# Kernel tuning notes

Hardware: AMD Instinct MI355X
Metric: run time of the kernel (lower is better)

## Reference

```python
import jax, jax.numpy as jnp
import numpy as np

N, E, IN_DIM, HID, HEADS = 50000, 400000, 128, 64, 4
NEG_SLOPE, LN_EPS = 0.2, 1e-5


def setup_inputs() -> dict:
    key = jax.random.key(0)
    ks = jax.random.split(key, 12)
    x = jax.random.normal(ks[0], (N, IN_DIM), dtype=jnp.float32)
    edge_index = jax.random.randint(ks[1], (2, E), 0, N, dtype=jnp.int64)
    s = 1.0 / np.sqrt(HID)
    return {
        "x": x,
        "edge_index": edge_index,
        "W_gcn": jax.random.normal(ks[2], (IN_DIM, HID), dtype=jnp.float32) / np.sqrt(IN_DIM),
        "b_gcn": jnp.zeros((HID,), dtype=jnp.float32),
        "W_gat": jax.random.normal(ks[3], (HID, HEADS * HID), dtype=jnp.float32) * s,
        "att_src": jax.random.normal(ks[4], (HEADS, HID), dtype=jnp.float32) * s,
        "att_dst": jax.random.normal(ks[5], (HEADS, HID), dtype=jnp.float32) * s,
        "b_gat": jnp.zeros((HID,), dtype=jnp.float32),
        "W_patch": jax.random.normal(ks[6], (HID, HID), dtype=jnp.float32) * s,
        "b_patch": jnp.zeros((HID,), dtype=jnp.float32),
        "gamma": jnp.ones((HID,), dtype=jnp.float32),
        "beta": jnp.zeros((HID,), dtype=jnp.float32),
    }


def _forward(x, edge_index, W_gcn, b_gcn, W_gat, att_src, att_dst, b_gat,
             W_patch, b_patch, gamma, beta):
    n = x.shape[0]
    loop = jnp.arange(n, dtype=edge_index.dtype)
    src = jnp.concatenate([edge_index[0], loop])  # self-loops appended (PyG default)
    dst = jnp.concatenate([edge_index[1], loop])

    # ---- GCNConv: symmetric degree normalization + scatter-add ----
    deg = jax.ops.segment_sum(jnp.ones_like(dst, dtype=jnp.float32), dst, num_segments=n)
    dinv = jnp.where(deg > 0, jax.lax.rsqrt(deg), 0.0)
    norm = dinv[src] * dinv[dst]  # [E+N]
    xw = x @ W_gcn  # [N,HID]
    h1 = jax.ops.segment_sum(xw[src] * norm[:, None], dst, num_segments=n) + b_gcn
    h1 = jax.nn.relu(h1)

    # ---- GATConv (heads=4, concat=False -> mean over heads) ----
    z = (h1 @ W_gat).reshape(n, HEADS, HID)  # [N,H,C]
    a_s = jnp.einsum('nhc,hc->nh', z, att_src)  # [N,H]
    a_d = jnp.einsum('nhc,hc->nh', z, att_dst)
    e = jax.nn.leaky_relu(a_s[src] + a_d[dst], negative_slope=NEG_SLOPE)  # [E+N,H]
    # segment-softmax over incoming edges per destination node
    m = jax.ops.segment_max(e, dst, num_segments=n)  # [N,H]
    ex = jnp.exp(e - m[dst])
    denom = jax.ops.segment_sum(ex, dst, num_segments=n)
    alpha = ex / denom[dst]  # [E+N,H]
    agg = jax.ops.segment_sum(z[src] * alpha[:, :, None], dst, num_segments=n)  # [N,H,C]
    h2 = jax.nn.relu(agg.mean(axis=1) + b_gat)

    # ---- residual fusion + LayerNorm (dropout is identity in eval) ----
    h_patch = h1 @ W_patch + b_patch
    h = h1 + h2 + h_patch
    mu = h.mean(axis=-1, keepdims=True)
    var = h.var(axis=-1, keepdims=True)
    return (h - mu) * jax.lax.rsqrt(var + LN_EPS) * gamma + beta


def reference(x, edge_index, W_gcn, b_gcn, W_gat, att_src, att_dst, b_gat,
              W_patch, b_patch, gamma, beta):
    return _forward(x, edge_index, W_gcn, b_gcn, W_gat, att_src, att_dst, b_gat,
                    W_patch, b_patch, gamma, beta)
```

## Files before the change

### kernel.cpp

```cpp
#include <hip/hip_runtime.h>
#include <math.h>

#define IN_DIM 128
#define HID 64
#define HEADS 4
#define NEG_SLOPE 0.2f
#define LN_EPS 1e-5f
#define ECAP 512

typedef short bf16x8 __attribute__((ext_vector_type(8)));
typedef float f32x4  __attribute__((ext_vector_type(4)));

__device__ inline unsigned short f2bf(float f) {
    unsigned u = __float_as_uint(f);
    u += 0x7fffu + ((u >> 16) & 1u);
    return (unsigned short)(u >> 16);
}
__device__ inline float bf2f(unsigned short s) {
    return __uint_as_float(((unsigned)s) << 16);
}
__device__ inline float leaky(float v) { return v > 0.0f ? v : NEG_SLOPE * v; }

__global__ void k_init_all(const unsigned long long* ei, int E, int n,
                           int* flag, int* hist,
                           const float* __restrict__ Wg, const float* __restrict__ Wp,
                           const float* __restrict__ Wgcn,
                           const float* __restrict__ att_s, const float* __restrict__ att_d,
                           unsigned short* __restrict__ Wt_post,
                           unsigned short* __restrict__ Wt_xw,
                           float* __restrict__ w_s, float* __restrict__ w_d) {
    int nzb = (n + 255) >> 8;
    int t = threadIdx.x;
    if ((int)blockIdx.x < nzb) {
        int i = blockIdx.x * 256 + t;
        if (i < n) hist[i] = 0;
        if (blockIdx.x == 0) {
            __shared__ int s_bad;
            if (t == 0) s_bad = 0;
            __syncthreads();
            int lim = E < 4096 ? E : 4096;
            int bad = 0;
            for (int k = t; k < lim; k += 256)
                if (ei[k] >= (unsigned long long)n) bad = 1;
            if (bad) s_bad = 1;
            __syncthreads();
            if (t == 0) *flag = s_bad ? 0 : 1;
        }
        return;
    }
    int role = blockIdx.x - nzb;
    if (role < 14) {
        int p = role * 256 + t;
        if (p < 2560) {
            int c = p & 63, kg = p >> 6;
            bf16x8 v;
#pragma unroll
            for (int j = 0; j < 8; j++) {
                int k = kg * 8 + j;
                float f;
                if (k < 256) f = 0.25f * Wg[(size_t)(k & 63) * 256 + (k >> 6) * 64 + c];
                else         f = Wp[(size_t)(k - 256) * 64 + c];
                v[j] = (short)f2bf(f);
            }
            *(bf16x8*)(&Wt_post[(size_t)p * 8]) = v;
        } else if (p < 2560 + 1024) {
            int q = p - 2560;
            int c = q & 63, kg = q >> 6;
            bf16x8 v;
#pragma unroll
            for (int j = 0; j < 8; j++)
                v[j] = (short)f2bf(Wgcn[(size_t)(kg * 8 + j) * 64 + c]);
            *(bf16x8*)(&Wt_xw[(size_t)q * 8]) = v;
        }
    } else {
        int h = t >> 6, k = t & 63;
        float ss = 0.0f, sd = 0.0f;
        for (int c = 0; c < HID; c++) {
            float w = Wg[(size_t)k * (HEADS * HID) + h * HID + c];
            ss += w * att_s[h * HID + c];
            sd += w * att_d[h * HID + c];
        }
        w_s[h * HID + k] = ss;
        w_d[h * HID + k] = sd;
    }
}

__global__ void k_hist(const void* ei, int E, const int* flag, int* hist) {
    int i = blockIdx.x * blockDim.x + threadIdx.x;
    if (i >= E) return;
    int is64 = *flag;
    int d;
    if (is64) d = (int)((const long long*)ei)[E + i];
    else      d = ((const int*)ei)[E + i];
    atomicAdd(&hist[d], 1);
}

__global__ __launch_bounds__(256) void k_scan1(const int* __restrict__ hist,
                                               int* __restrict__ tmp,
                                               int* __restrict__ partial, int n) {
    __shared__ int s[256];
    int t = threadIdx.x, i = blockIdx.x * 256 + t;
    int v = (i < n) ? hist[i] : 0;
    s[t] = v;
    __syncthreads();
    for (int off = 1; off < 256; off <<= 1) {
        int x = (t >= off) ? s[t - off] : 0;
        __syncthreads();
        s[t] += x;
        __syncthreads();
    }
    tmp[i] = s[t] - v;
    if (t == 255) partial[blockIdx.x] = s[255];
}

__global__ __launch_bounds__(256) void k_scan_apply(const int* __restrict__ tmp,
                                                    const int* __restrict__ partial,
                                                    const int* __restrict__ hist,
                                                    int* __restrict__ row_ptr,
                                                    int* __restrict__ cursor,
                                                    float* __restrict__ dinv,
                                                    int n, int nscan) {
    __shared__ int s[256];
    __shared__ int excl_s;
    int t = threadIdx.x;
    int v = (t < nscan) ? partial[t] : 0;
    s[t] = v;
    __syncthreads();
    for (int off = 1; off < 256; off <<= 1) {
        int x = (t >= off) ? s[t - off] : 0;
        __syncthreads();
        s[t] += x;
        __syncthreads();
    }
    if (t == 0) excl_s = (blockIdx.x == 0) ? 0 : s[blockIdx.x - 1];
    __syncthreads();
    int excl = excl_s;
    int i = blockIdx.x * 256 + t;
    if (i < n) {
        int v2 = tmp[i] + excl;
        row_ptr[i] = v2;
        cursor[i] = v2;
        dinv[i] = rsqrtf((float)(hist[i] + 1));
    }
}

__global__ __launch_bounds__(256) void k_scatter_xw(const void* ei, int E,
                                                    const int* __restrict__ flag,
                                                    int* __restrict__ cursor,
                                                    int* __restrict__ col,
                                                    const float* __restrict__ x,
                                                    const unsigned short* __restrict__ Wt_g,
                                                    const float* __restrict__ dinv,
                                                    unsigned short* __restrict__ xws, int n) {
    __shared__ unsigned short Wt[16 * 64 * 8];
    int nsb = (E + 255) >> 8;
    if ((int)blockIdx.x < nsb) {
        int i = blockIdx.x * 256 + threadIdx.x;
        if (i >= E) return;
        int is64 = *flag;
        int s, d;
        if (is64) { s = (int)((const long long*)ei)[i]; d = (int)((const long long*)ei)[E + i]; }
        else      { s = ((const int*)ei)[i];            d = ((const int*)ei)[E + i]; }
        int pos = atomicAdd(&cursor[d], 1);
        col[pos] = s;
    } else {
        int bx = blockIdx.x - nsb;
        int t = threadIdx.x;
        for (int idx = t; idx < 1024; idx += 256)
            *(bf16x8*)(&Wt[idx * 8]) = *(const bf16x8*)(&Wt_g[(size_t)idx * 8]);
        __syncthreads();
        int lane = t & 63;
        int li = lane & 15, quad = lane >> 4;
        int w = t >> 6;
        int r0 = bx * 64 + w * 16;
        int rload = r0 + li; if (rload > n - 1) rload = n - 1;
        f32x4 acc[4];
#pragma unroll
        for (int i = 0; i < 4; i++) acc[i] = (f32x4){0.f, 0.f, 0.f, 0.f};
        const float* xp = x + (size_t)rload * IN_DIM + quad * 8;
#pragma unroll
        for (int ks = 0; ks < 4; ks++) {
            float4 p0 = *(const float4*)(xp + ks * 32);
            float4 p1 = *(const float4*)(xp + ks * 32 + 4);
            bf16x8 a;
            a[0] = (short)f2bf(p0.x); a[1] = (short)f2bf(p0.y);
            a[2] = (short)f2bf(p0.z); a[3] = (short)f2bf(p0.w);
            a[4] = (short)f2bf(p1.x); a[5] = (short)f2bf(p1.y);
            a[6] = (short)f2bf(p1.z); a[7] = (short)f2bf(p1.w);
            int kg = ks * 4 + quad;
#pragma unroll
            for (int tt = 0; tt < 4; tt++) {
                bf16x8 bfr = *(const bf16x8*)(&Wt[((kg * 64) + tt * 16 + li) * 8]);
                acc[tt] = __builtin_amdgcn_mfma_f32_16x16x32_bf16(a, bfr, acc[tt], 0, 0, 0);
            }
        }
#pragma unroll
        for (int reg = 0; reg < 4; reg++) {
            int r = r0 + quad * 4 + reg;
            if (r >= n) continue;
            float dv = dinv[r];
#pragma unroll
            for (int tt = 0; tt < 4; tt++)
                xws[(size_t)r * HID + tt * 16 + li] = f2bf(acc[tt][reg] * dv);
        }
    }
}

__global__ __launch_bounds__(256) void k_gcn(const int* __restrict__ col,
                                             const int* __restrict__ row_ptr,
                                             const int* __restrict__ hist,
                                             const float* __restrict__ dinv,
                                             const unsigned short* __restrict__ xws,
                                             const float* __restrict__ b,
                                             const float* __restrict__ w_s,
                                             const float* __restrict__ w_d,
                                             unsigned short* __restrict__ h1b,
                                             float4* __restrict__ a_s,
                                             float4* __restrict__ a_d, int n) {
    int t = threadIdx.x, c = t & 63;
    int d = blockIdx.x * 4 + (t >> 6);
    if (d >= n) return;
    int start = row_ptr[d], cnt = hist[d];
    float acc = bf2f(xws[(size_t)d * HID + c]);
    int k = 0;
    for (; k + 3 < cnt; k += 4) {
        int s0 = col[start + k],     s1 = col[start + k + 1];
        int s2 = col[start + k + 2], s3 = col[start + k + 3];
        float v0 = bf2f(xws[(size_t)s0 * HID + c]);
        float v1 = bf2f(xws[(size_t)s1 * HID + c]);
        float v2 = bf2f(xws[(size_t)s2 * HID + c]);
        float v3 = bf2f(xws[(size_t)s3 * HID + c]);
        acc += (v0 + v1) + (v2 + v3);
    }
    for (; k < cnt; k++) acc += bf2f(xws[(size_t)col[start + k] * HID + c]);
    float h1c = fmaxf(acc * dinv[d] + b[c], 0.0f);
    h1b[(size_t)d * HID + c] = f2bf(h1c);
    float vs0 = h1c * w_s[c],       vs1 = h1c * w_s[64 + c];
    float vs2 = h1c * w_s[128 + c], vs3 = h1c * w_s[192 + c];
    float vd0 = h1c * w_d[c],       vd1 = h1c * w_d[64 + c];
    float vd2 = h1c * w_d[128 + c], vd3 = h1c * w_d[192 + c];
    for (int o = 32; o > 0; o >>= 1) {
        vs0 += __shfl_xor(vs0, o, 64); vs1 += __shfl_xor(vs1, o, 64);
        vs2 += __shfl_xor(vs2, o, 64); vs3 += __shfl_xor(vs3, o, 64);
        vd0 += __shfl_xor(vd0, o, 64); vd1 += __shfl_xor(vd1, o, 64);
        vd2 += __shfl_xor(vd2, o, 64); vd3 += __shfl_xor(vd3, o, 64);
    }
    if (c == 0) {
        a_s[d] = make_float4(vs0, vs1, vs2, vs3);
        a_d[d] = make_float4(vd0, vd1, vd2, vd3);
    }
}

__global__ __launch_bounds__(256) void k_attn(const int* __restrict__ col,
                                              const int* __restrict__ row_ptr,
                                              const int* __restrict__ hist,
                                              const float4* __restrict__ a_s,
                                              const float4* __restrict__ a_d,
                                              const unsigned short* __restrict__ h1b,
                                              unsigned short* __restrict__ X, int n) {
    __shared__ float4 wls[ECAP];
    __shared__ int    sls[ECAP];
    __shared__ int    sb[5];
    __shared__ float4 sad[4];
    int t = threadIdx.x;
    int d0 = blockIdx.x * 4;
    if (t == 0) {
        int bptr = row_ptr[d0];
        sb[0] = bptr;
        for (int j = 0; j < 4; j++) {
            int d = d0 + j;
            bptr += (d < n) ? hist[d] : 0;
            sb[j + 1] = bptr;
        }
    }
    if (t < 4 && d0 + t < n) sad[t] = a_d[d0 + t];
    __syncthreads();
    int start0 = sb[0];
    int totc = sb[4] - start0;
    int rel1 = sb[1] - start0, rel2 = sb[2] - start0, rel3 = sb[3] - start0;
    bool fast = (totc <= ECAP);
    if (fast) {
        for (int e = t; e < totc; e += 256) {
            int s = col[start0 + e];
            int j = (e >= rel1) + (e >= rel2) + (e >= rel3);
            float4 as = a_s[s], ad = sad[j];
            float4 w;
            w.x = __expf(leaky(as.x + ad.x));
            w.y = __expf(leaky(as.y + ad.y));
            w.z = __expf(leaky(as.z + ad.z));
            w.w = __expf(leaky(as.w + ad.w));
            wls[e] = w;
            sls[e] = s;
        }
    }
    __syncthreads();
    int c = t & 63, w = t >> 6;
    int d = d0 + w;
    if (d >= n) return;
    float4 ad = sad[w];
    float4 asd = a_s[d];
    float w0 = __expf(leaky(asd.x + ad.x));
    float w1 = __expf(leaky(asd.y + ad.y));
    float w2 = __expf(leaky(asd.z + ad.z));
    float w3 = __expf(leaky(asd.w + ad.w));
    float hs = bf2f(h1b[(size_t)d * HID + c]);
    float A0 = w0 * hs, A1 = w1 * hs, A2 = w2 * hs, A3 = w3 * hs;
    float l0 = w0, l1 = w1, l2 = w2, l3 = w3;
    int lo = sb[w] - start0, hi = sb[w + 1] - start0;
    if (fast) {
        int k = lo;
        for (; k + 3 < hi; k += 4) {
            int s0 = sls[k], s1 = sls[k + 1], s2 = sls[k + 2], s3 = sls[k + 3];
            float4 e0 = wls[k], e1 = wls[k + 1], e2 = wls[k + 2], e3 = wls[k + 3];
            float hv0 = bf2f(h1b[(size_t)s0 * HID + c]);
            float hv1 = bf2f(h1b[(size_t)s1 * HID + c]);
            float hv2 = bf2f(h1b[(size_t)s2 * HID + c]);
            float hv3 = bf2f(h1b[(size_t)s3 * HID + c]);
            A0 += e0.x * hv0 + e1.x * hv1 + e2.x * hv2 + e3.x * hv3;
            A1 += e0.y * hv0 + e1.y * hv1 + e2.y * hv2 + e3.y * hv3;
            A2 += e0.z * hv0 + e1.z * hv1 + e2.z * hv2 + e3.z * hv3;
            A3 += e0.w * hv0 + e1.w * hv1 + e2.w * hv2 + e3.w * hv3;
            l0 += (e0.x + e1.x) + (e2.x + e3.x);
            l1 += (e0.y + e1.y) + (e2.y + e3.y);
            l2 += (e0.z + e1.z) + (e2.z + e3.z);
            l3 += (e0.w + e1.w) + (e2.w + e3.w);
        }
        for (; k < hi; k++) {
            int s0 = sls[k];
            float4 e0 = wls[k];
            float hv0 = bf2f(h1b[(size_t)s0 * HID + c]);
            A0 += e0.x * hv0; l0 += e0.x;
            A1 += e0.y * hv0; l1 += e0.y;
            A2 += e0.z * hv0; l2 += e0.z;
            A3 += e0.w * hv0; l3 += e0.w;
        }
    } else {
        for (int k = lo; k < hi; k++) {
            int s0 = col[start0 + k];
            float4 as = a_s[s0];
            float u0 = __expf(leaky(as.x + ad.x));
            float u1 = __expf(leaky(as.y + ad.y));
            float u2 = __expf(leaky(as.z + ad.z));
            float u3 = __expf(leaky(as.w + ad.w));
            float hv0 = bf2f(h1b[(size_t)s0 * HID + c]);
            A0 += u0 * hv0; l0 += u0;
            A1 += u1 * hv0; l1 += u1;
            A2 += u2 * hv0; l2 += u2;
            A3 += u3 * hv0; l3 += u3;
        }
    }
    size_t base = (size_t)d * 256;
    X[base + c]       = f2bf(A0 / l0);
    X[base + 64 + c]  = f2bf(A1 / l1);
    X[base + 128 + c] = f2bf(A2 / l2);
    X[base + 192 + c] = f2bf(A3 / l3);
}

__global__ __launch_bounds__(256) void k_post(const unsigned short* __restrict__ Wt_g,
                                              const unsigned short* __restrict__ X,
                                              const unsigned short* __restrict__ h1b,
                                              const float* __restrict__ bp,
                                              const float* __restrict__ bg,
                                              const float* __restrict__ gamma,
                                              const float* __restrict__ beta,
                                              float* __restrict__ out, int n) {
    __shared__ unsigned short Wt[2560 * 8];
    int t = threadIdx.x;
    for (int idx = t; idx < 2560; idx += 256)
        *(bf16x8*)(&Wt[idx * 8]) = *(const bf16x8*)(&Wt_g[(size_t)idx * 8]);
    __syncthreads();

    int lane = t & 63;
    int li = lane & 15, quad = lane >> 4;
    int w = t >> 6;
    int rbase = blockIdx.x * 128 + w * 32;

    f32x4 acc_a[2][4], acc_h[2][4];
#pragma unroll
    for (int rt = 0; rt < 2; rt++)
#pragma unroll
        for (int i = 0; i < 4; i++) {
            acc_a[rt][i] = (f32x4){0.f, 0.f, 0.f, 0.f};
            acc_h[rt][i] = (f32x4){0.f, 0.f, 0.f, 0.f};
        }
#pragma unroll
    for (int ks = 0; ks < 10; ks++) {
        int kg = ks * 4 + quad;
        bf16x8 b0 = *(const bf16x8*)(&Wt[((kg * 64) + 0 * 16 + li) * 8]);
        bf16x8 b1 = *(const bf16x8*)(&Wt[((kg * 64) + 1 * 16 + li) * 8]);
        bf16x8 b2 = *(const bf16x8*)(&Wt[((kg * 64) + 2 * 16 + li) * 8]);
        bf16x8 b3 = *(const bf16x8*)(&Wt[((kg * 64) + 3 * 16 + li) * 8]);
#pragma unroll
        for (int rt = 0; rt < 2; rt++) {
            int row = rbase + rt * 16 + li;
            bf16x8 a;
            if (ks < 8)
                a = *(const bf16x8*)(X + (size_t)row * 256 + quad * 8 + ks * 32);
            else
                a = *(const bf16x8*)(h1b + (size_t)row * HID + quad * 8 + (ks - 8) * 32);
            if (ks < 8) {
                acc_a[rt][0] = __builtin_amdgcn_mfma_f32_16x16x32_bf16(a, b0, acc_a[rt][0], 0, 0, 0);
                acc_a[rt][1] = __builtin_amdgcn_mfma_f32_16x16x32_bf16(a, b1, acc_a[rt][1], 0, 0, 0);
                acc_a[rt][2] = __builtin_amdgcn_mfma_f32_16x16x32_bf16(a, b2, acc_a[rt][2], 0, 0, 0);
                acc_a[rt][3] = __builtin_amdgcn_mfma_f32_16x16x32_bf16(a, b3, acc_a[rt][3], 0, 0, 0);
            } else {
                acc_h[rt][0] = __builtin_amdgcn_mfma_f32_16x16x32_bf16(a, b0, acc_h[rt][0], 0, 0, 0);
                acc_h[rt][1] = __builtin_amdgcn_mfma_f32_16x16x32_bf16(a, b1, acc_h[rt][1], 0, 0, 0);
                acc_h[rt][2] = __builtin_amdgcn_mfma_f32_16x16x32_bf16(a, b2, acc_h[rt][2], 0, 0, 0);
                acc_h[rt][3] = __builtin_amdgcn_mfma_f32_16x16x32_bf16(a, b3, acc_h[rt][3], 0, 0, 0);
            }
        }
    }
    float bgv[4], bpv[4], gv[4], btv[4];
#pragma unroll
    for (int tt = 0; tt < 4; tt++) {
        int c = tt * 16 + li;
        bgv[tt] = bg[c]; bpv[tt] = bp[c]; gv[tt] = gamma[c]; btv[tt] = beta[c];
    }
#pragma unroll
    for (int rt = 0; rt < 2; rt++) {
#pragma unroll
        for (int reg = 0; reg < 4; reg++) {
            int r = rbase + rt * 16 + quad * 4 + reg;
            bool ok = (r < n);
            float hv[4];
            float s1 = 0.0f, s2 = 0.0f;
#pragma unroll
            for (int tt = 0; tt < 4; tt++) {
                int c = tt * 16 + li;
                float h1c = ok ? bf2f(h1b[(size_t)r * HID + c]) : 0.0f;
                float h2 = fmaxf(acc_a[rt][tt][reg] + bgv[tt], 0.0f);
                float h = h1c + h2 + acc_h[rt][tt][reg] + bpv[tt];
                hv[tt] = h;
                s1 += h; s2 += h * h;
            }
            for (int o = 8; o > 0; o >>= 1) {
                s1 += __shfl_xor(s1, o, 64);
                s2 += __shfl_xor(s2, o, 64);
            }
            float mu = s1 * (1.0f / 64.0f);
            float var = s2 * (1.0f / 64.0f) - mu * mu;
            float rs = rsqrtf(var + LN_EPS);
            if (ok) {
#pragma unroll
                for (int tt = 0; tt < 4; tt++) {
                    int c = tt * 16 + li;
                    out[(size_t)r * HID + c] = (hv[tt] - mu) * rs * gv[tt] + btv[tt];
                }
            }
        }
    }
}

extern "C" void kernel_launch(void* const* d_in, const int* in_sizes, int n_in,
                              void* d_out, int out_size, void* d_ws, size_t ws_size,
                              hipStream_t stream) {
    int n = in_sizes[0] / IN_DIM;
    int E = in_sizes[1] / 2;

    const float* x     = (const float*)d_in[0];
    const void*  ei    = d_in[1];
    const float* W_gcn = (const float*)d_in[2];
    const float* b_gcn = (const float*)d_in[3];
    const float* W_gat = (const float*)d_in[4];
    const float* att_s = (const float*)d_in[5];
    const float* att_d = (const float*)d_in[6];
    const float* b_gat = (const float*)d_in[7];
    const float* W_p   = (const float*)d_in[8];
    const float* b_p   = (const float*)d_in[9];
    const float* gamma = (const float*)d_in[10];
    const float* beta  = (const float*)d_in[11];

    int n_pad  = ((n + 255) / 256) * 256;
    int nscan  = n_pad / 256;
    int n128   = ((n + 127) / 128) * 128;
    int nzb    = (n + 255) / 256;
    int nsb    = (E + 255) / 256;

    float* ws = (float*)d_ws;
    size_t off = 0;
    int*   flag    = (int*)(ws + off);  off += 4;
    int*   hist    = (int*)(ws + off);  off += n;
    int*   row_ptr = (int*)(ws + off);  off += n;
    int*   cursor  = (int*)(ws + off);  off += n;
    int*   tmp     = (int*)(ws + off);  off += n_pad;
    int*   partial = (int*)(ws + off);  off += 256;
    int*   colv    = (int*)(ws + off);  off += E;
    float* dinv    = ws + off;          off += n;
    float* w_s     = ws + off;          off += HEADS * HID;
    float* w_d     = ws + off;          off += HEADS * HID;
    off = (off + 3) & ~(size_t)3;
    unsigned short* Wt_post = (unsigned short*)(ws + off); off += 2560 * 8 / 2;
    unsigned short* Wt_xw   = (unsigned short*)(ws + off); off += 1024 * 8 / 2;
    unsigned short* xws = (unsigned short*)(ws + off); off += (size_t)n * HID / 2;
    off = (off + 3) & ~(size_t)3;
    unsigned short* h1b = (unsigned short*)(ws + off); off += (size_t)n128 * HID / 2;
    off = (off + 3) & ~(size_t)3;
    float4* a_sv   = (float4*)(ws + off); off += (size_t)n * 4;
    float4* a_dv   = (float4*)(ws + off); off += (size_t)n * 4;
    off = (off + 3) & ~(size_t)3;
    unsigned short* X = (unsigned short*)(ws + off); off += (size_t)n128 * 256 / 2;

    k_init_all<<<nzb + 15, 256, 0, stream>>>((const unsigned long long*)ei, E, n,
                                             flag, hist, W_gat, W_p, W_gcn,
                                             att_s, att_d, Wt_post, Wt_xw, w_s, w_d);
    k_hist<<<nsb, 256, 0, stream>>>(ei, E, flag, hist);

    k_scan1<<<nscan, 256, 0, stream>>>(hist, tmp, partial, n);
    k_scan_apply<<<nscan, 256, 0, stream>>>(tmp, partial, hist, row_ptr, cursor,
                                            dinv, n, nscan);

    k_scatter_xw<<<nsb + (n + 63) / 64, 256, 0, stream>>>(ei, E, flag, cursor,
                                                          colv, x, Wt_xw,
                                                          dinv, xws, n);

    k_gcn<<<(n + 3) / 4, 256, 0, stream>>>(colv, row_ptr, hist, dinv, xws, b_gcn,
                                           w_s, w_d, h1b, a_sv, a_dv, n);

    k_attn<<<(n + 3) / 4, 256, 0, stream>>>(colv, row_ptr, hist, a_sv, a_dv,
                                            h1b, X, n);

    k_post<<<(n + 127) / 128, 256, 0, stream>>>(Wt_post, X, h1b, b_p, b_gat,
                                                gamma, beta, (float*)d_out, n);
}
```

Measured before the change: 226.0 us.

## Fuse all stages into one cooperative persistent kernel with grid syncs

Replaces the eight separate kernel launches (init, histogram, two scan passes, scatter plus xw GEMM, GCN gather, attention, post GEMM plus LayerNorm) with one cooperative kernel. It uses grid-stride loops over work items and grid-wide barriers between stages. The aim is to remove launch overhead and inter-kernel gaps. The cost is a grid capped by occupancy, a fixed 40KB shared buffer that may reduce occupancy, and per-phase grid syncs. Load balance may also suffer in the gather stages.

```diff
diff --git a/kernel.cpp b/kernel.cpp
--- a/kernel.cpp
+++ b/kernel.cpp
@@ -1,9 +1,11 @@
 #include <hip/hip_runtime.h>
+#include <hip/hip_cooperative_groups.h>
 #include <math.h>
+
+namespace cg = cooperative_groups;
 
 #define IN_DIM 128
 #define HID 64
-#define HEADS 4
 #define NEG_SLOPE 0.2f
 #define LN_EPS 1e-5f
 #define ECAP 512
@@ -21,36 +23,29 @@
 }
 __device__ inline float leaky(float v) { return v > 0.0f ? v : NEG_SLOPE * v; }
 
-__global__ void k_init_all(const unsigned long long* ei, int E, int n,
-                           int* flag, int* hist,
-                           const float* __restrict__ Wg, const float* __restrict__ Wp,
-                           const float* __restrict__ Wgcn,
-                           const float* __restrict__ att_s, const float* __restrict__ att_d,
-                           unsigned short* __restrict__ Wt_post,
-                           unsigned short* __restrict__ Wt_xw,
-                           float* __restrict__ w_s, float* __restrict__ w_d) {
-    int nzb = (n + 255) >> 8;
+__global__ __launch_bounds__(256, 4) void k_mega(
+    const unsigned long long* ei64, int E, int n, int nscan,
+    int* flag, int* hist, int* tmp, int* partial,
+    int* row_ptr, int* cursor, int* col,
+    const float* x, const float* bgcn,
+    const float* Wg, const float* att_s, const float* att_d,
+    const float* Wp, const float* Wgcn,
+    const float* bp, const float* bg,
+    const float* gamma, const float* beta,
+    unsigned short* Wt_post, unsigned short* Wt_xw,
+    float* w_s, float* w_d, float* dinv,
+    unsigned short* xws, unsigned short* h1b,
+    float4* a_s, float4* a_d,
+    unsigned short* X, float* out)
+{
+    cg::grid_group gridg = cg::this_grid();
+    __shared__ __align__(16) unsigned char smem[40960];
     int t = threadIdx.x;
-    if ((int)blockIdx.x < nzb) {
-        int i = blockIdx.x * 256 + t;
-        if (i < n) hist[i] = 0;
-        if (blockIdx.x == 0) {
-            __shared__ int s_bad;
-            if (t == 0) s_bad = 0;
-            __syncthreads();
-            int lim = E < 4096 ? E : 4096;
-            int bad = 0;
-            for (int k = t; k < lim; k += 256)
-                if (ei[k] >= (unsigned long long)n) bad = 1;
-            if (bad) s_bad = 1;
-            __syncthreads();
-            if (t == 0) *flag = s_bad ? 0 : 1;
-        }
-        return;
-    }
-    int role = blockIdx.x - nzb;
-    if (role < 14) {
-        int p = role * 256 + t;
+    int gtid = blockIdx.x * 256 + t;
+    int gstride = gridDim.x * 256;
+
+    for (int i = gtid; i < n; i += gstride) hist[i] = 0;
+    for (int p = gtid; p < 2560 + 1024 + 256; p += gstride) {
         if (p < 2560) {
             int c = p & 63, kg = p >> 6;
             bf16x8 v;
@@ -63,7 +58,7 @@
                 v[j] = (short)f2bf(f);
             }
             *(bf16x8*)(&Wt_post[(size_t)p * 8]) = v;
-        } else if (p < 2560 + 1024) {
+        } else if (p < 3584) {
             int q = p - 2560;
             int c = q & 63, kg = q >> 6;
             bf16x8 v;
@@ -71,381 +66,357 @@
             for (int j = 0; j < 8; j++)
                 v[j] = (short)f2bf(Wgcn[(size_t)(kg * 8 + j) * 64 + c]);
             *(bf16x8*)(&Wt_xw[(size_t)q * 8]) = v;
-        }
-    } else {
-        int h = t >> 6, k = t & 63;
-        float ss = 0.0f, sd = 0.0f;
-        for (int c = 0; c < HID; c++) {
-            float w = Wg[(size_t)k * (HEADS * HID) + h * HID + c];
-            ss += w * att_s[h * HID + c];
-            sd += w * att_d[h * HID + c];
-        }
-        w_s[h * HID + k] = ss;
-        w_d[h * HID + k] = sd;
-    }
-}
-
-__global__ void k_hist(const void* ei, int E, const int* flag, int* hist) {
-    int i = blockIdx.x * blockDim.x + threadIdx.x;
-    if (i >= E) return;
+        } else {
+            int q = p - 3584;
+            int h = q >> 6, k = q & 63;
+            float ss = 0.0f, sd = 0.0f;
+            for (int c = 0; c < HID; c++) {
+                float w = Wg[(size_t)k * 256 + h * HID + c];
+                ss += w * att_s[h * HID + c];
+                sd += w * att_d[h * HID + c];
+            }
+            w_s[h * HID + k] = ss;
+            w_d[h * HID + k] = sd;
+        }
+    }
+    if (blockIdx.x == 0) {
+        int* s_bad = (int*)smem;
+        if (t == 0) *s_bad = 0;
+        __syncthreads();
+        int lim = E < 4096 ? E : 4096;
+        int bad = 0;
+        for (int k = t; k < lim; k += 256)
+            if (ei64[k] >= (unsigned long long)n) bad = 1;
+        if (bad) *s_bad = 1;
+        __syncthreads();
+        if (t == 0) *flag = (*s_bad) ? 0 : 1;
+    }
+    gridg.sync();
+
     int is64 = *flag;
-    int d;
-    if (is64) d = (int)((const long long*)ei)[E + i];
-    else      d = ((const int*)ei)[E + i];
-    atomicAdd(&hist[d], 1);
-}
-
-__global__ __launch_bounds__(256) void k_scan1(const int* __restrict__ hist,
-                                               int* __restrict__ tmp,
-                                               int* __restrict__ partial, int n) {
-    __shared__ int s[256];
-    int t = threadIdx.x, i = blockIdx.x * 256 + t;
-    int v = (i < n) ? hist[i] : 0;
-    s[t] = v;
-    __syncthreads();
-    for (int off = 1; off < 256; off <<= 1) {
-        int x = (t >= off) ? s[t - off] : 0;
+    const long long* e64 = (const long long*)ei64;
+    const int* e32 = (const int*)ei64;
+
+    for (int i = gtid; i < E; i += gstride) {
+        int d = is64 ? (int)e64[E + i] : e32[E + i];
+        atomicAdd(&hist[d], 1);
+    }
+    gridg.sync();
+
+    {
+        int* s = (int*)smem;
+        for (int cb = blockIdx.x; cb < nscan; cb += gridDim.x) {
+            int i = cb * 256 + t;
+            int v = (i < n) ? hist[i] : 0;
+            s[t] = v;
+            __syncthreads();
+            for (int off = 1; off < 256; off <<= 1) {
+                int xv = (t >= off) ? s[t - off] : 0;
+                __syncthreads();
+                s[t] += xv;
+                __syncthreads();
+            }
+            tmp[i] = s[t] - v;
+            if (t == 255) partial[cb] = s[255];
+            __syncthreads();
+        }
+    }
+    gridg.sync();
+
+    {
+        int* s = (int*)smem;
+        int v = (t < nscan) ? partial[t] : 0;
+        s[t] = v;
         __syncthreads();
-        s[t] += x;
+        for (int off = 1; off < 256; off <<= 1) {
+            int xv = (t >= off) ? s[t - off] : 0;
+            __syncthreads();
+            s[t] += xv;
+            __syncthreads();
+        }
+        for (int cb = blockIdx.x; cb < nscan; cb += gridDim.x) {
+            int excl = (cb == 0) ? 0 : s[cb - 1];
+            int i = cb * 256 + t;
+            if (i < n) {
+                int v2 = tmp[i] + excl;
+                row_ptr[i] = v2;
+                cursor[i] = v2;
+                dinv[i] = rsqrtf((float)(hist[i] + 1));
+            }
+        }
         __syncthreads();
     }
-    tmp[i] = s[t] - v;
-    if (t == 255) partial[blockIdx.x] = s[255];
-}
-
-__global__ __launch_bounds__(256) void k_scan_apply(const int* __restrict__ tmp,
-                                                    const int* __restrict__ partial,
-                                                    const int* __restrict__ hist,
-                                                    int* __restrict__ row_ptr,
-                                                    int* __restrict__ cursor,
-                                                    float* __restrict__ dinv,
-                                                    int n, int nscan) {
-    __shared__ int s[256];
-    __shared__ int excl_s;
-    int t = threadIdx.x;
-    int v = (t < nscan) ? partial[t] : 0;
-    s[t] = v;
-    __syncthreads();
-    for (int off = 1; off < 256; off <<= 1) {
-        int x = (t >= off) ? s[t - off] : 0;
+    gridg.sync();
+
+    for (int i = gtid; i < E; i += gstride) {
+        int sn = is64 ? (int)e64[i] : e32[i];
+        int d = is64 ? (int)e64[E + i] : e32[E + i];
+        int pos = atomicAdd(&cursor[d], 1);
+        col[pos] = sn;
+    }
+    {
+        unsigned short* Wt = (unsigned short*)smem;
+        for (int idx = t; idx < 1024; idx += 256)
+            *(bf16x8*)(&Wt[idx * 8]) = *(const bf16x8*)(&Wt_xw[(size_t)idx * 8]);
         __syncthreads();
-        s[t] += x;
+        int lane = t & 63, li = lane & 15, quad = lane >> 4, wv = t >> 6;
+        int ntile = (n + 63) / 64;
+        for (int tile = blockIdx.x; tile < ntile; tile += gridDim.x) {
+            int r0 = tile * 64 + wv * 16;
+            int rload = r0 + li; if (rload > n - 1) rload = n - 1;
+            f32x4 acc[4];
+#pragma unroll
+            for (int i = 0; i < 4; i++) acc[i] = (f32x4){0.f, 0.f, 0.f, 0.f};
+            const float* xp = x + (size_t)rload * IN_DIM + quad * 8;
+#pragma unroll
+            for (int ks = 0; ks < 4; ks++) {
+                float4 p0 = *(const float4*)(xp + ks * 32);
+                float4 p1 = *(const float4*)(xp + ks * 32 + 4);
+                bf16x8 a;
+                a[0] = (short)f2bf(p0.x); a[1] = (short)f2bf(p0.y);
+                a[2] = (short)f2bf(p0.z); a[3] = (short)f2bf(p0.w);
+                a[4] = (short)f2bf(p1.x); a[5] = (short)f2bf(p1.y);
+                a[6] = (short)f2bf(p1.z); a[7] = (short)f2bf(p1.w);
+                int kg = ks * 4 + quad;
+#pragma unroll
+                for (int tt = 0; tt < 4; tt++) {
+                    bf16x8 bfr = *(const bf16x8*)(&Wt[((kg * 64) + tt * 16 + li) * 8]);
+                    acc[tt] = __builtin_amdgcn_mfma_f32_16x16x32_bf16(a, bfr, acc[tt], 0, 0, 0);
+                }
+            }
+#pragma unroll
+            for (int reg = 0; reg < 4; reg++) {
+                int r = r0 + quad * 4 + reg;
+                if (r >= n) continue;
+                float dv = dinv[r];
+#pragma unroll
+                for (int tt = 0; tt < 4; tt++)
+                    xws[(size_t)r * HID + tt * 16 + li] = f2bf(acc[tt][reg] * dv);
+            }
+        }
+    }
+    gridg.sync();
+
+    {
+        int c = t & 63, wv = t >> 6;
+        int ndb = (n + 3) / 4;
+        for (int db = blockIdx.x; db < ndb; db += gridDim.x) {
+            int d = db * 4 + wv;
+            if (d < n) {
+                int start = row_ptr[d], cnt = hist[d];
+                float acc = bf2f(xws[(size_t)d * HID + c]);
+                int k = 0;
+                for (; k + 3 < cnt; k += 4) {
+                    int s0 = col[start + k],     s1 = col[start + k + 1];
+                    int s2 = col[start + k + 2], s3 = col[start + k + 3];
+                    float v0 = bf2f(xws[(size_t)s0 * HID + c]);
+                    float v1 = bf2f(xws[(size_t)s1 * HID + c]);
+                    float v2 = bf2f(xws[(size_t)s2 * HID + c]);
+                    float v3 = bf2f(xws[(size_t)s3 * HID + c]);
+                    acc += (v0 + v1) + (v2 + v3);
+                }
+                for (; k < cnt; k++) acc += bf2f(xws[(size_t)col[start + k] * HID + c]);
+                float h1c = fmaxf(acc * dinv[d] + bgcn[c], 0.0f);
+                h1b[(size_t)d * HID + c] = f2bf(h1c);
+                float vs0 = h1c * w_s[c],       vs1 = h1c * w_s[64 + c];
+                float vs2 = h1c * w_s[128 + c], vs3 = h1c * w_s[192 + c];
+                float vd0 = h1c * w_d[c],       vd1 = h1c * w_d[64 + c];
+                float vd2 = h1c * w_d[128 + c], vd3 = h1c * w_d[192 + c];
+                for (int o = 32; o > 0; o >>= 1) {
+                    vs0 += __shfl_xor(vs0, o, 64); vs1 += __shfl_xor(vs1, o, 64);
+                    vs2 += __shfl_xor(vs2, o, 64); vs3 += __shfl_xor(vs3, o, 64);
+                    vd0 += __shfl_xor(vd0, o, 64); vd1 += __shfl_xor(vd1, o, 64);
+                    vd2 += __shfl_xor(vd2, o, 64); vd3 += __shfl_xor(vd3, o, 64);
+                }
+                if (c == 0) {
+                    a_s[d] = make_float4(vs0, vs1, vs2, vs3);
+                    a_d[d] = make_float4(vd0, vd1, vd2, vd3);
+                }
+            }
+        }
+    }
+    gridg.sync();
+
+    {
+        float4* wls = (float4*)smem;
+        int*    sls = (int*)(smem + 8192);
+        int*    sb  = (int*)(smem + 10240);
+        float4* sad = (float4*)(smem + 10272);
+        int ndb = (n + 3) / 4;
+        for (int db = blockIdx.x; db < ndb; db += gridDim.x) {
+            int d0 = db * 4;
+            if (t == 0) {
+                int bptr = row_ptr[d0];
+                sb[0] = bptr;
+                for (int j = 0; j < 4; j++) {
+                    int d = d0 + j;
+                    bptr += (d < n) ? hist[d] : 0;
+                    sb[j + 1] = bptr;
+                }
+            }
+            if (t < 4 && d0 + t < n) sad[t] = a_d[d0 + t];
+            __syncthreads();
+            int start0 = sb[0];
+            int totc = sb[4] - start0;
+            int rel1 = sb[1] - start0, rel2 = sb[2] - start0, rel3 = sb[3] - start0;
+            bool fast = (totc <= ECAP);
+            if (fast) {
+                for (int e = t; e < totc; e += 256) {
+                    int s = col[start0 + e];
+                    int j = (e >= rel1) + (e >= rel2) + (e >= rel3);
+                    float4 as = a_s[s], ad = sad[j];
+                    float4 wv4;
+                    wv4.x = __expf(leaky(as.x + ad.x));
+                    wv4.y = __expf(leaky(as.y + ad.y));
+                    wv4.z = __expf(leaky(as.z + ad.z));
+                    wv4.w = __expf(leaky(as.w + ad.w));
+                    wls[e] = wv4;
+                    sls[e] = s;
+                }
+            }
+            __syncthreads();
+            int c = t & 63, wv = t >> 6;
+            int d = d0 + wv;
+            if (d < n) {
+                float4 ad = sad[wv];
+                float4 asd = a_s[d];
+                float w0 = __expf(leaky(asd.x + ad.x));
+                float w1 = __expf(leaky(asd.y + ad.y));
+                float w2 = __expf(leaky(asd.z + ad.z));
+                float w3 = __expf(leaky(asd.w + ad.w));
+                float hs = bf2f(h1b[(size_t)d * HID + c]);
+                float A0 = w0 * hs, A1 = w1 * hs, A2 = w2 * hs, A3 = w3 * hs;
+                float l0 = w0, l1 = w1, l2 = w2, l3 = w3;
+                int lo = sb[wv] - start0, hi = sb[wv + 1] - start0;
+                if (fast) {
+                    int k = lo;
+                    for (; k + 3 < hi; k += 4) {
+                        int s0 = sls[k], s1 = sls[k + 1], s2 = sls[k + 2], s3 = sls[k + 3];
+                        float4 e0 = wls[k], e1 = wls[k + 1], e2 = wls[k + 2], e3 = wls[k + 3];
+                        float hv0 = bf2f(h1b[(size_t)s0 * HID + c]);
+                        float hv1 = bf2f(h1b[(size_t)s1 * HID + c]);
+                        float hv2 = bf2f(h1b[(size_t)s2 * HID + c]);
+                        float hv3 = bf2f(h1b[(size_t)s3 * HID + c]);
+                        A0 += e0.x * hv0 + e1.x * hv1 + e2.x * hv2 + e3.x * hv3;
+                        A1 += e0.y * hv0 + e1.y * hv1 + e2.y * hv2 + e3.y * hv3;
+                        A2 += e0.z * hv0 + e1.z * hv1 + e2.z * hv2 + e3.z * hv3;
+                        A3 += e0.w * hv0 + e1.w * hv1 + e2.w * hv2 + e3.w * hv3;
+                        l0 += (e0.x + e1.x) + (e2.x + e3.x);
+                        l1 += (e0.y + e1.y) + (e2.y + e3.y);
+                        l2 += (e0.z + e1.z) + (e2.z + e3.z);
+                        l3 += (e0.w + e1.w) + (e2.w + e3.w);
+                    }
+                    for (; k < hi; k++) {
+                        int s0 = sls[k];
+                        float4 e0 = wls[k];
+                        float hv0 = bf2f(h1b[(size_t)s0 * HID + c]);
+                        A0 += e0.x * hv0; l0 += e0.x;
+                        A1 += e0.y * hv0; l1 += e0.y;
+                        A2 += e0.z * hv0; l2 += e0.z;
+                        A3 += e0.w * hv0; l3 += e0.w;
+                    }
+                } else {
+                    for (int k = lo; k < hi; k++) {
+                        int s0 = col[start0 + k];
+                        float4 as = a_s[s0];
+                        float u0 = __expf(leaky(as.x + ad.x));
+                        float u1 = __expf(leaky(as.y + ad.y));
+                        float u2 = __expf(leaky(as.z + ad.z));
+                        float u3 = __expf(leaky(as.w + ad.w));
+                        float hv0 = bf2f(h1b[(size_t)s0 * HID + c]);
+                        A0 += u0 * hv0; l0 += u0;
+                        A1 += u1 * hv0; l1 += u1;
+                        A2 += u2 * hv0; l2 += u2;
+                        A3 += u3 * hv0; l3 += u3;
+                    }
+                }
+                size_t base = (size_t)d * 256;
+                X[base + c]       = f2bf(A0 / l0);
+                X[base + 64 + c]  = f2bf(A1 / l1);
+                X[base + 128 + c] = f2bf(A2 / l2);
+                X[base + 192 + c] = f2bf(A3 / l3);
+            }
+            __syncthreads();
+        }
+    }
+    gridg.sync();
+
+    {
+        unsigned short* Wt = (unsigned short*)smem;
+        for (int idx = t; idx < 2560; idx += 256)
+            *(bf16x8*)(&Wt[idx * 8]) = *(const bf16x8*)(&Wt_post[(size_t)idx * 8]);
         __syncthreads();
-    }
-    if (t == 0) excl_s = (blockIdx.x == 0) ? 0 : s[blockIdx.x - 1];
-    __syncthreads();
-    int excl = excl_s;
-    int i = blockIdx.x * 256 + t;
-    if (i < n) {
-        int v2 = tmp[i] + excl;
-        row_ptr[i] = v2;
-        cursor[i] = v2;
-        dinv[i] = rsqrtf((float)(hist[i] + 1));
-    }
-}
-
-__global__ __launch_bounds__(256) void k_scatter_xw(const void* ei, int E,
-                                                    const int* __restrict__ flag,
-                                                    int* __restrict__ cursor,
-                                                    int* __restrict__ col,
-                                                    const float* __restrict__ x,
-                                                    const unsigned short* __restrict__ Wt_g,
-                                                    const float* __restrict__ dinv,
-                                                    unsigned short* __restrict__ xws, int n) {
-    __shared__ unsigned short Wt[16 * 64 * 8];
-    int nsb = (E + 255) >> 8;
-    if ((int)blockIdx.x < nsb) {
-        int i = blockIdx.x * 256 + threadIdx.x;
-        if (i >= E) return;
-        int is64 = *flag;
-        int s, d;
-        if (is64) { s = (int)((const long long*)ei)[i]; d = (int)((const long long*)ei)[E + i]; }
-        else      { s = ((const int*)ei)[i];            d = ((const int*)ei)[E + i]; }
-        int pos = atomicAdd(&cursor[d], 1);
-        col[pos] = s;
-    } else {
-        int bx = blockIdx.x - nsb;
-        int t = threadIdx.x;
-        for (int idx = t; idx < 1024; idx += 256)
-            *(bf16x8*)(&Wt[idx * 8]) = *(const bf16x8*)(&Wt_g[(size_t)idx * 8]);
-        __syncthreads();
-        int lane = t & 63;
-        int li = lane & 15, quad = lane >> 4;
-        int w = t >> 6;
-        int r0 = bx * 64 + w * 16;
-        int rload = r0 + li; if (rload > n - 1) rload = n - 1;
-        f32x4 acc[4];
-#pragma unroll
-        for (int i = 0; i < 4; i++) acc[i] = (f32x4){0.f, 0.f, 0.f, 0.f};
-        const float* xp = x + (size_t)rload * IN_DIM + quad * 8;
-#pragma unroll
-        for (int ks = 0; ks < 4; ks++) {
-            float4 p0 = *(const float4*)(xp + ks * 32);
-            float4 p1 = *(const float4*)(xp + ks * 32 + 4);
-            bf16x8 a;
-            a[0] = (short)f2bf(p0.x); a[1] = (short)f2bf(p0.y);
-            a[2] = (short)f2bf(p0.z); a[3] = (short)f2bf(p0.w);
-            a[4] = (short)f2bf(p1.x); a[5] = (short)f2bf(p1.y);
-            a[6] = (short)f2bf(p1.z); a[7] = (short)f2bf(p1.w);
-            int kg = ks * 4 + quad;
-#pragma unroll
-            for (int tt = 0; tt < 4; tt++) {
-                bf16x8 bfr = *(const bf16x8*)(&Wt[((kg * 64) + tt * 16 + li) * 8]);
-                acc[tt] = __builtin_amdgcn_mfma_f32_16x16x32_bf16(a, bfr, acc[tt], 0, 0, 0);
-            }
-        }
-#pragma unroll
-        for (int reg = 0; reg < 4; reg++) {
-            int r = r0 + quad * 4 + reg;
-            if (r >= n) continue;
-            float dv = dinv[r];
-#pragma unroll
-            for (int tt = 0; tt < 4; tt++)
-                xws[(size_t)r * HID + tt * 16 + li] = f2bf(acc[tt][reg] * dv);
-        }
-    }
-}
-
-__global__ __launch_bounds__(256) void k_gcn(const int* __restrict__ col,
-                                             const int* __restrict__ row_ptr,
-                                             const int* __restrict__ hist,
-                                             const float* __restrict__ dinv,
-                                             const unsigned short* __restrict__ xws,
-                                             const float* __restrict__ b,
-                                             const float* __restrict__ w_s,
-                                             const float* __restrict__ w_d,
-                                             unsigned short* __restrict__ h1b,
-                                             float4* __restrict__ a_s,
-                                             float4* __restrict__ a_d, int n) {
-    int t = threadIdx.x, c = t & 63;
-    int d = blockIdx.x * 4 + (t >> 6);
-    if (d >= n) return;
-    int start = row_ptr[d], cnt = hist[d];
-    float acc = bf2f(xws[(size_t)d * HID + c]);
-    int k = 0;
-    for (; k + 3 < cnt; k += 4) {
-        int s0 = col[start + k],     s1 = col[start + k + 1];
-        int s2 = col[start + k + 2], s3 = col[start + k + 3];
-        float v0 = bf2f(xws[(size_t)s0 * HID + c]);
-        float v1 = bf2f(xws[(size_t)s1 * HID + c]);
-        float v2 = bf2f(xws[(size_t)s2 * HID + c]);
-        float v3 = bf2f(xws[(size_t)s3 * HID + c]);
-        acc += (v0 + v1) + (v2 + v3);
-    }
-    for (; k < cnt; k++) acc += bf2f(xws[(size_t)col[start + k] * HID + c]);
-    float h1c = fmaxf(acc * dinv[d] + b[c], 0.0f);
-    h1b[(size_t)d * HID + c] = f2bf(h1c);
-    float vs0 = h1c * w_s[c],       vs1 = h1c * w_s[64 + c];
-    float vs2 = h1c * w_s[128 + c], vs3 = h1c * w_s[192 + c];
-    float vd0 = h1c * w_d[c],       vd1 = h1c * w_d[64 + c];
-    float vd2 = h1c * w_d[128 + c], vd3 = h1c * w_d[192 + c];
-    for (int o = 32; o > 0; o >>= 1) {
-        vs0 += __shfl_xor(vs0, o, 64); vs1 += __shfl_xor(vs1, o, 64);
-        vs2 += __shfl_xor(vs2, o, 64); vs3 += __shfl_xor(vs3, o, 64);
-        vd0 += __shfl_xor(vd0, o, 64); vd1 += __shfl_xor(vd1, o, 64);
-        vd2 += __shfl_xor(vd2, o, 64); vd3 += __shfl_xor(vd3, o, 64);
-    }
-    if (c == 0) {
-        a_s[d] = make_float4(vs0, vs1, vs2, vs3);
-        a_d[d] = make_float4(vd0, vd1, vd2, vd3);
-    }
-}
-
-__global__ __launch_bounds__(256) void k_attn(const int* __restrict__ col,
-                                              const int* __restrict__ row_ptr,
-                                              const int* __restrict__ hist,
-                                              const float4* __restrict__ a_s,
-                                              const float4* __restrict__ a_d,
-                                              const unsigned short* __restrict__ h1b,
-                                              unsigned short* __restrict__ X, int n) {
-    __shared__ float4 wls[ECAP];
-    __shared__ int    sls[ECAP];
-    __shared__ int    sb[5];
-    __shared__ float4 sad[4];
-    int t = threadIdx.x;
-    int d0 = blockIdx.x * 4;
-    if (t == 0) {
-        int bptr = row_ptr[d0];
-        sb[0] = bptr;
-        for (int j = 0; j < 4; j++) {
-            int d = d0 + j;
-            bptr += (d < n) ? hist[d] : 0;
-            sb[j + 1] = bptr;
-        }
-    }
-    if (t < 4 && d0 + t < n) sad[t] = a_d[d0 + t];
-    __syncthreads();
-    int start0 = sb[0];
-    int totc = sb[4] - start0;
-    int rel1 = sb[1] - start0, rel2 = sb[2] - start0, rel3 = sb[3] - start0;
-    bool fast = (totc <= ECAP);
-    if (fast) {
-        for (int e = t; e < totc; e += 256) {
-            int s = col[start0 + e];
-            int j = (e >= rel1) + (e >= rel2) + (e >= rel3);
-            float4 as = a_s[s], ad = sad[j];
-            float4 w;
-            w.x = __expf(leaky(as.x + ad.x));
-            w.y = __expf(leaky(as.y + ad.y));
-            w.z = __expf(leaky(as.z + ad.z));
-            w.w = __expf(leaky(as.w + ad.w));
-            wls[e] = w;
-            sls[e] = s;
-        }
-    }
-    __syncthreads();
-    int c = t & 63, w = t >> 6;
-    int d = d0 + w;
-    if (d >= n) return;
-    float4 ad = sad[w];
-    float4 asd = a_s[d];
-    float w0 = __expf(leaky(asd.x + ad.x));
-    float w1 = __expf(leaky(asd.y + ad.y));
-    float w2 = __expf(leaky(asd.z + ad.z));
-    float w3 = __expf(leaky(asd.w + ad.w));
-    float hs = bf2f(h1b[(size_t)d * HID + c]);
-    float A0 = w0 * hs, A1 = w1 * hs, A2 = w2 * hs, A3 = w3 * hs;
-    float l0 = w0, l1 = w1, l2 = w2, l3 = w3;
-    int lo = sb[w] - start0, hi = sb[w + 1] - start0;
-    if (fast) {
-        int k = lo;
-        for (; k + 3 < hi; k += 4) {
-            int s0 = sls[k], s1 = sls[k + 1], s2 = sls[k + 2], s3 = sls[k + 3];
-            float4 e0 = wls[k], e1 = wls[k + 1], e2 = wls[k + 2], e3 = wls[k + 3];
-            float hv0 = bf2f(h1b[(size_t)s0 * HID + c]);
-            float hv1 = bf2f(h1b[(size_t)s1 * HID + c]);
-            float hv2 = bf2f(h1b[(size_t)s2 * HID + c]);
-            float hv3 = bf2f(h1b[(size_t)s3 * HID + c]);
-            A0 += e0.x * hv0 + e1.x * hv1 + e2.x * hv2 + e3.x * hv3;
-            A1 += e0.y * hv0 + e1.y * hv1 + e2.y * hv2 + e3.y * hv3;
-            A2 += e0.z * hv0 + e1.z * hv1 + e2.z * hv2 + e3.z * hv3;
-            A3 += e0.w * hv0 + e1.w * hv1 + e2.w * hv2 + e3.w * hv3;
-            l0 += (e0.x + e1.x) + (e2.x + e3.x);
-            l1 += (e0.y + e1.y) + (e2.y + e3.y);
-            l2 += (e0.z + e1.z) + (e2.z + e3.z);
-            l3 += (e0.w + e1.w) + (e2.w + e3.w);
-        }
-        for (; k < hi; k++) {
-            int s0 = sls[k];
-            float4 e0 = wls[k];
-            float hv0 = bf2f(h1b[(size_t)s0 * HID + c]);
-            A0 += e0.x * hv0; l0 += e0.x;
-            A1 += e0.y * hv0; l1 += e0.y;
-            A2 += e0.z * hv0; l2 += e0.z;
-            A3 += e0.w * hv0; l3 += e0.w;
-        }
-    } else {
-        for (int k = lo; k < hi; k++) {
-            int s0 = col[start0 + k];
-            float4 as = a_s[s0];
-            float u0 = __expf(leaky(as.x + ad.x));
-            float u1 = __expf(leaky(as.y + ad.y));
-            float u2 = __expf(leaky(as.z + ad.z));
-            float u3 = __expf(leaky(as.w + ad.w));
-            float hv0 = bf2f(h1b[(size_t)s0 * HID + c]);
-            A0 += u0 * hv0; l0 += u0;
-            A1 += u1 * hv0; l1 += u1;
-            A2 += u2 * hv0; l2 += u2;
-            A3 += u3 * hv0; l3 += u3;
-        }
-    }
-    size_t base = (size_t)d * 256;
-    X[base + c]       = f2bf(A0 / l0);
-    X[base + 64 + c]  = f2bf(A1 / l1);
-    X[base + 128 + c] = f2bf(A2 / l2);
-    X[base + 192 + c] = f2bf(A3 / l3);
-}
-
-__global__ __launch_bounds__(256) void k_post(const unsigned short* __restrict__ Wt_g,
-                                              const unsigned short* __restrict__ X,
-                                              const unsigned short* __restrict__ h1b,
-                                              const float* __restrict__ bp,
-                                              const float* __restrict__ bg,
-                                              const float* __restrict__ gamma,
-                                              const float* __restrict__ beta,
-                                              float* __restrict__ out, int n) {
-    __shared__ unsigned short Wt[2560 * 8];
-    int t = threadIdx.x;
-    for (int idx = t; idx < 2560; idx += 256)
-        *(bf16x8*)(&Wt[idx * 8]) = *(const bf16x8*)(&Wt_g[(size_t)idx * 8]);
-    __syncthreads();
-
-    int lane = t & 63;
-    int li = lane & 15, quad = lane >> 4;
-    int w = t >> 6;
-    int rbase = blockIdx.x * 128 + w * 32;
-
-    f32x4 acc_a[2][4], acc_h[2][4];
-#pragma unroll
-    for (int rt = 0; rt < 2; rt++)
-#pragma unroll
-        for (int i = 0; i < 4; i++) {
-            acc_a[rt][i] = (f32x4){0.f, 0.f, 0.f, 0.f};
-            acc_h[rt][i] = (f32x4){0.f, 0.f, 0.f, 0.f};
-        }
-#pragma unroll
-    for (int ks = 0; ks < 10; ks++) {
-        int kg = ks * 4 + quad;
-        bf16x8 b0 = *(const bf16x8*)(&Wt[((kg * 64) + 0 * 16 + li) * 8]);
-        bf16x8 b1 = *(const bf16x8*)(&Wt[((kg * 64) + 1 * 16 + li) * 8]);
-        bf16x8 b2 = *(const bf16x8*)(&Wt[((kg * 64) + 2 * 16 + li) * 8]);
-        bf16x8 b3 = *(const bf16x8*)(&Wt[((kg * 64) + 3 * 16 + li) * 8]);
-#pragma unroll
-        for (int rt = 0; rt < 2; rt++) {
-            int row = rbase + rt * 16 + li;
-            bf16x8 a;
-            if (ks < 8)
-                a = *(const bf16x8*)(X + (size_t)row * 256 + quad * 8 + ks * 32);
-            else
-                a = *(const bf16x8*)(h1b + (size_t)row * HID + quad * 8 + (ks - 8) * 32);
-            if (ks < 8) {
-                acc_a[rt][0] = __builtin_amdgcn_mfma_f32_16x16x32_bf16(a, b0, acc_a[rt][0], 0, 0, 0);
-                acc_a[rt][1] = __builtin_amdgcn_mfma_f32_16x16x32_bf16(a, b1, acc_a[rt][1], 0, 0, 0);
-                acc_a[rt][2] = __builtin_amdgcn_mfma_f32_16x16x32_bf16(a, b2, acc_a[rt][2], 0, 0, 0);
-                acc_a[rt][3] = __builtin_amdgcn_mfma_f32_16x16x32_bf16(a, b3, acc_a[rt][3], 0, 0, 0);
-            } else {
-                acc_h[rt][0] = __builtin_amdgcn_mfma_f32_16x16x32_bf16(a, b0, acc_h[rt][0], 0, 0, 0);
-                acc_h[rt][1] = __builtin_amdgcn_mfma_f32_16x16x32_bf16(a, b1, acc_h[rt][1], 0, 0, 0);
-                acc_h[rt][2] = __builtin_amdgcn_mfma_f32_16x16x32_bf16(a, b2, acc_h[rt][2], 0, 0, 0);
-                acc_h[rt][3] = __builtin_amdgcn_mfma_f32_16x16x32_bf16(a, b3, acc_h[rt][3], 0, 0, 0);
-            }
-        }
-    }
-    float bgv[4], bpv[4], gv[4], btv[4];
-#pragma unroll
-    for (int tt = 0; tt < 4; tt++) {
-        int c = tt * 16 + li;
-        bgv[tt] = bg[c]; bpv[tt] = bp[c]; gv[tt] = gamma[c]; btv[tt] = beta[c];
-    }
-#pragma unroll
-    for (int rt = 0; rt < 2; rt++) {
-#pragma unroll
-        for (int reg = 0; reg < 4; reg++) {
-            int r = rbase + rt * 16 + quad * 4 + reg;
-            bool ok = (r < n);
-            float hv[4];
-            float s1 = 0.0f, s2 = 0.0f;
-#pragma unroll
-            for (int tt = 0; tt < 4; tt++) {
-                int c = tt * 16 + li;
-                float h1c = ok ? bf2f(h1b[(size_t)r * HID + c]) : 0.0f;
-                float h2 = fmaxf(acc_a[rt][tt][reg] + bgv[tt], 0.0f);
-                float h = h1c + h2 + acc_h[rt][tt][reg] + bpv[tt];
-                hv[tt] = h;
-                s1 += h; s2 += h * h;
-            }
-            for (int o = 8; o > 0; o >>= 1) {
-                s1 += __shfl_xor(s1, o, 64);
-                s2 += __shfl_xor(s2, o, 64);
-            }
-            float mu = s1 * (1.0f / 64.0f);
-            float var = s2 * (1.0f / 64.0f) - mu * mu;
-            float rs = rsqrtf(var + LN_EPS);
-            if (ok) {
-#pragma unroll
-                for (int tt = 0; tt < 4; tt++) {
-                    int c = tt * 16 + li;
-                    out[(size_t)r * HID + c] = (hv[tt] - mu) * rs * gv[tt] + btv[tt];
+        int lane = t & 63, li = lane & 15, quad = lane >> 4, wv = t >> 6;
+        int ntile = (n + 127) / 128;
+        for (int tile = blockIdx.x; tile < ntile; tile += gridDim.x) {
+            int rbase = tile * 128 + wv * 32;
+            f32x4 acc_a[2][4], acc_h[2][4];
+#pragma unroll
+            for (int rt = 0; rt < 2; rt++)
+#pragma unroll
+                for (int i = 0; i < 4; i++) {
+                    acc_a[rt][i] = (f32x4){0.f, 0.f, 0.f, 0.f};
+                    acc_h[rt][i] = (f32x4){0.f, 0.f, 0.f, 0.f};
+                }
+#pragma unroll
+            for (int ks = 0; ks < 10; ks++) {
+                int kg = ks * 4 + quad;
+                bf16x8 b0 = *(const bf16x8*)(&Wt[((kg * 64) + 0 * 16 + li) * 8]);
+                bf16x8 b1 = *(const bf16x8*)(&Wt[((kg * 64) + 1 * 16 + li) * 8]);
+                bf16x8 b2 = *(const bf16x8*)(&Wt[((kg * 64) + 2 * 16 + li) * 8]);
+                bf16x8 b3 = *(const bf16x8*)(&Wt[((kg * 64) + 3 * 16 + li) * 8]);
+#pragma unroll
+                for (int rt = 0; rt < 2; rt++) {
+                    int row = rbase + rt * 16 + li;
+                    bf16x8 a;
+                    if (ks < 8)
+                        a = *(const bf16x8*)(X + (size_t)row * 256 + quad * 8 + ks * 32);
+                    else
+                        a = *(const bf16x8*)(h1b + (size_t)row * HID + quad * 8 + (ks - 8) * 32);
+                    if (ks < 8) {
+                        acc_a[rt][0] = __builtin_amdgcn_mfma_f32_16x16x32_bf16(a, b0, acc_a[rt][0], 0, 0, 0);
+                        acc_a[rt][1] = __builtin_amdgcn_mfma_f32_16x16x32_bf16(a, b1, acc_a[rt][1], 0, 0, 0);
+                        acc_a[rt][2] = __builtin_amdgcn_mfma_f32_16x16x32_bf16(a, b2, acc_a[rt][2], 0, 0, 0);
+                        acc_a[rt][3] = __builtin_amdgcn_mfma_f32_16x16x32_bf16(a, b3, acc_a[rt][3], 0, 0, 0);
+                    } else {
+                        acc_h[rt][0] = __builtin_amdgcn_mfma_f32_16x16x32_bf16(a, b0, acc_h[rt][0], 0, 0, 0);
+                        acc_h[rt][1] = __builtin_amdgcn_mfma_f32_16x16x32_bf16(a, b1, acc_h[rt][1], 0, 0, 0);
+                        acc_h[rt][2] = __builtin_amdgcn_mfma_f32_16x16x32_bf16(a, b2, acc_h[rt][2], 0, 0, 0);
+                        acc_h[rt][3] = __builtin_amdgcn_mfma_f32_16x16x32_bf16(a, b3, acc_h[rt][3], 0, 0, 0);
+                    }
+                }
+            }
+#pragma unroll
+            for (int rt = 0; rt < 2; rt++) {
+#pragma unroll
+                for (int reg = 0; reg < 4; reg++) {
+                    int r = rbase + rt * 16 + quad * 4 + reg;
+                    bool ok = (r < n);
+                    float hv[4];
+                    float s1 = 0.0f, s2 = 0.0f;
+#pragma unroll
+                    for (int tt = 0; tt < 4; tt++) {
+                        int c = tt * 16 + li;
+                        float h1c = ok ? bf2f(h1b[(size_t)r * HID + c]) : 0.0f;
+                        float h2 = fmaxf(acc_a[rt][tt][reg] + bg[c], 0.0f);
+                        float h = h1c + h2 + acc_h[rt][tt][reg] + bp[c];
+                        hv[tt] = h;
+                        s1 += h; s2 += h * h;
+                    }
+                    for (int o = 8; o > 0; o >>= 1) {
+                        s1 += __shfl_xor(s1, o, 64);
+                        s2 += __shfl_xor(s2, o, 64);
+                    }
+                    float mu = s1 * (1.0f / 64.0f);
+                    float var = s2 * (1.0f / 64.0f) - mu * mu;
+                    float rs = rsqrtf(var + LN_EPS);
+                    if (ok) {
+#pragma unroll
+                        for (int tt = 0; tt < 4; tt++) {
+                            int c = tt * 16 + li;
+                            out[(size_t)r * HID + c] = (hv[tt] - mu) * rs * gamma[c] + beta[c];
+                        }
+                    }
                 }
             }
         }
@@ -474,8 +445,6 @@
     int n_pad  = ((n + 255) / 256) * 256;
     int nscan  = n_pad / 256;
     int n128   = ((n + 127) / 128) * 128;
-    int nzb    = (n + 255) / 256;
-    int nsb    = (E + 255) / 256;
 
     float* ws = (float*)d_ws;
     size_t off = 0;
@@ -487,8 +456,8 @@
     int*   partial = (int*)(ws + off);  off += 256;
     int*   colv    = (int*)(ws + off);  off += E;
     float* dinv    = ws + off;          off += n;
-    float* w_s     = ws + off;          off += HEADS * HID;
-    float* w_d     = ws + off;          off += HEADS * HID;
+    float* w_s     = ws + off;          off += 4 * HID;
+    float* w_d     = ws + off;          off += 4 * HID;
     off = (off + 3) & ~(size_t)3;
     unsigned short* Wt_post = (unsigned short*)(ws + off); off += 2560 * 8 / 2;
     unsigned short* Wt_xw   = (unsigned short*)(ws + off); off += 1024 * 8 / 2;
@@ -501,25 +470,31 @@
     off = (off + 3) & ~(size_t)3;
     unsigned short* X = (unsigned short*)(ws + off); off += (size_t)n128 * 256 / 2;
 
-    k_init_all<<<nzb + 15, 256, 0, stream>>>((const unsigned long long*)ei, E, n,
-                                             flag, hist, W_gat, W_p, W_gcn,
-                                             att_s, att_d, Wt_post, Wt_xw, w_s, w_d);
-    k_hist<<<nsb, 256, 0, stream>>>(ei, E, flag, hist);
-
-    k_scan1<<<nscan, 256, 0, stream>>>(hist, tmp, partial, n);
-    k_scan_apply<<<nscan, 256, 0, stream>>>(tmp, partial, hist, row_ptr, cursor,
-                                            dinv, n, nscan);
-
-    k_scatter_xw<<<nsb + (n + 63) / 64, 256, 0, stream>>>(ei, E, flag, cursor,
-                                                          colv, x, Wt_xw,
-                                                          dinv, xws, n);
-
-    k_gcn<<<(n + 3) / 4, 256, 0, stream>>>(colv, row_ptr, hist, dinv, xws, b_gcn,
-                                           w_s, w_d, h1b, a_sv, a_dv, n);
-
-    k_attn<<<(n + 3) / 4, 256, 0, stream>>>(colv, row_ptr, hist, a_sv, a_dv,
-                                            h1b, X, n);
-
-    k_post<<<(n + 127) / 128, 256, 0, stream>>>(Wt_post, X, h1b, b_p, b_gat,
-                                                gamma, beta, (float*)d_out, n);
+    int maxB = 0;
+    if (hipOccupancyMaxActiveBlocksPerMultiprocessor(&maxB, (const void*)k_mega,
+                                                     256, 0) != hipSuccess || maxB < 1)
+        maxB = 2;
+    long long gridLL = (long long)maxB * 256;
+    if (gridLL > 2048) gridLL = 2048;
+    int grid = (int)gridLL;
+
+    const unsigned long long* ei64 = (const unsigned long long*)ei;
+    float* outp = (float*)d_out;
+    void* args[] = {
+        (void*)&ei64, (void*)&E, (void*)&n, (void*)&nscan,
+        (void*)&flag, (void*)&hist, (void*)&tmp, (void*)&partial,
+        (void*)&row_ptr, (void*)&cursor, (void*)&colv,
+        (void*)&x, (void*)&b_gcn,
+        (void*)&W_gat, (void*)&att_s, (void*)&att_d,
+        (void*)&W_p, (void*)&W_gcn,
+        (void*)&b_p, (void*)&b_gat,
+        (void*)&gamma, (void*)&beta,
+        (void*)&Wt_post, (void*)&Wt_xw,
+        (void*)&w_s, (void*)&w_d, (void*)&dinv,
+        (void*)&xws, (void*)&h1b,
+        (void*)&a_sv, (void*)&a_dv,
+        (void*)&X, (void*)&outp
+    };
+    hipLaunchCooperativeKernel((const void*)k_mega, dim3(grid), dim3(256),
+                               args, 0, stream);
 }
```

After: 772.2 us. +241.7%, slower.
